# Kernel optimization log

Hardware: AMD Instinct MI355X
Metric: run time of the kernel (lower is better)

## Reference

```python
import jax, jax.numpy as jnp
import numpy as np

N, D = 256, 512
DIST_W, ANGLE_W = 1.0, 2.0
EPS_PD = 1e-6    # F.pairwise_distance eps (added to the difference)
EPS_COS = 1e-8   # F.cosine_similarity eps (denominator floor)
CLAMP = 1e-7     # acos clamp margin


def _smooth_l1(x):
    # F.smooth_l1_loss with beta=1.0, elementwise (reduction handled by caller)
    ax = jnp.abs(x)
    return jnp.where(ax < 1.0, 0.5 * ax * ax, ax - 0.5)


def _pairwise_dist(E):
    # Faithful to the looped version: dist[i,j] = ||e_i - e_j + eps|| for i<j,
    # mirrored to the lower triangle, zero diagonal.
    diff = E[:, None, :] - E[None, :, :] + EPS_PD          # [n, n, d]
    d = jnp.sqrt(jnp.sum(diff * diff, axis=-1))            # [n, n]
    upper = jnp.triu(d, k=1)
    return upper + upper.T


def _angles(E):
    # ang[j, i, k] = angle at vertex j between (e_i - e_j) and (e_k - e_j)
    Dv = E[None, :, :] - E[:, None, :]                     # Dv[j, a] = e_a - e_j
    norms = jnp.sqrt(jnp.sum(Dv * Dv, axis=-1))            # [n, n]
    dots = jnp.einsum('jad,jbd->jab', Dv, Dv)              # [n, n, n]
    denom = jnp.maximum(norms[:, :, None] * norms[:, None, :], EPS_COS)
    cos = jnp.clip(dots / denom, -1.0 + CLAMP, 1.0 - CLAMP)
    return jnp.arccos(cos)


def setup_inputs() -> dict:
    key = jax.random.key(0)
    k1, k2 = jax.random.split(key)
    return {
        'student_embeddings': jax.random.normal(k1, (N, D), dtype=jnp.float32),
        'teacher_embeddings': jax.random.normal(k2, (N, D), dtype=jnp.float32),
    }


def reference(student_embeddings, teacher_embeddings):
    # distance-wise loss: smooth_l1 mean over the full n x n matrix
    ds = _pairwise_dist(student_embeddings)
    dt = _pairwise_dist(teacher_embeddings)
    distance_loss = jnp.mean(_smooth_l1(ds - dt))

    # angle-wise loss: mean over triplets i<j<k (vertex at j)
    n = student_embeddings.shape[0]
    ang_s = _angles(student_embeddings)
    ang_t = _angles(teacher_embeddings)
    idx = jnp.arange(n)
    # mask[j, i, k] = (i < j) & (j < k)
    mask = (idx[None, :, None] < idx[:, None, None]) & (idx[:, None, None] < idx[None, None, :])
    count = n * (n - 1) * (n - 2) // 6
    angle_loss = jnp.sum(_smooth_l1(ang_s - ang_t) * mask) / count

    total_loss = DIST_W * distance_loss + ANGLE_W * angle_loss
    return (total_loss, distance_loss, angle_loss)
```

## Files before the change

kernel.cpp:

```cpp
#include <hip/hip_runtime.h>
#include <math.h>

#define N 256
#define D 512


__global__ void gram_kernel(const float* __restrict__ Es,
                            const float* __restrict__ Et,
                            float* __restrict__ Gs,
                            float* __restrict__ Gt) {
    const float* E = blockIdx.z ? Et : Es;
    float* G = blockIdx.z ? Gt : Gs;
    __shared__ float As[16][17];
    __shared__ float Bs[16][17];
    const int tx = threadIdx.x, ty = threadIdx.y;
    const int row = blockIdx.y * 16 + ty;
    const int colr = blockIdx.x * 16 + ty;
    float acc = 0.f;
    for (int k0 = 0; k0 < D; k0 += 16) {
        As[ty][tx] = E[row * D + k0 + tx];
        Bs[ty][tx] = E[colr * D + k0 + tx];
        __syncthreads();
#pragma unroll
        for (int kk = 0; kk < 16; ++kk)
            acc += As[ty][kk] * Bs[tx][kk];
        __syncthreads();
    }
    G[row * N + blockIdx.x * 16 + tx] = acc;
}

__global__ void rowsum_kernel(const float* __restrict__ Es,
                              const float* __restrict__ Et,
                              float* __restrict__ Ss,
                              float* __restrict__ St) {
    const float* E = blockIdx.y ? Et : Es;
    float* S = blockIdx.y ? St : Ss;
    const int row = blockIdx.x;
    const int t = threadIdx.x;
    float s = 0.f;
    for (int d = t; d < D; d += 64) s += E[row * D + d];
#pragma unroll
    for (int off = 32; off > 0; off >>= 1) s += __shfl_down(s, off);
    if (t == 0) S[row] = s;
}

__device__ __forceinline__ float smooth_l1(float x) {
    float ax = fabsf(x);
    return ax < 1.f ? 0.5f * ax * ax : ax - 0.5f;
}

__global__ void dist_kernel(const float* __restrict__ Gs,
                            const float* __restrict__ Gt,
                            const float* __restrict__ Ss,
                            const float* __restrict__ St,
                            float* __restrict__ acc) {
    const int i = blockIdx.x;
    const int j = threadIdx.x;
    float v = 0.f;
    if (i < j) {
        const float epsc = (float)((double)D * 1e-12);
        float ds2 = Gs[i * N + i] - 2.f * Gs[i * N + j] + Gs[j * N + j]
                    + 2e-6f * (Ss[i] - Ss[j]) + epsc;
        float dt2 = Gt[i * N + i] - 2.f * Gt[i * N + j] + Gt[j * N + j]
                    + 2e-6f * (St[i] - St[j]) + epsc;
        v = smooth_l1(sqrtf(ds2) - sqrtf(dt2));
    }
    __shared__ float red[256];
    red[j] = v;
    __syncthreads();
    for (int s = 128; s > 0; s >>= 1) {
        if (j < s) red[j] += red[j + s];
        __syncthreads();
    }
    if (j == 0) atomicAdd(&acc[0], red[0]);
}

__global__ void angle_kernel(const float* __restrict__ Gs,
                             const float* __restrict__ Gt,
                             float* __restrict__ acc) {
    const int j = blockIdx.x + 1;
    const int tid = threadIdx.x;
    __shared__ float cs[N], ct[N], rns[N], rnt[N];
    const float Gsjj = Gs[j * N + j];
    const float Gtjj = Gt[j * N + j];

    {
        float cja = Gs[tid * N + j];
        float cjb = Gt[tid * N + j];
        cs[tid] = cja;
        ct[tid] = cjb;
        float n2s = Gs[tid * N + tid] - 2.f * cja + Gsjj;
        float n2t = Gt[tid * N + tid] - 2.f * cjb + Gtjj;
        rns[tid] = (tid == j) ? 0.f : 1.f / sqrtf(n2s);
        rnt[tid] = (tid == j) ? 0.f : 1.f / sqrtf(n2t);
    }
    __syncthreads();

    const int nk = 255 - j;
    const int npairs = j * nk;
    const float lo = (float)(-1.0 + 1e-7);
    const float hi = (float)(1.0 - 1e-7);

    float partial = 0.f;
    for (int p = tid; p < npairs; p += 256) {
        int i = p / nk;
        int k = j + 1 + (p - i * nk);
        float dots = Gs[i * N + k] - cs[i] - cs[k] + Gsjj;
        float dott = Gt[i * N + k] - ct[i] - ct[k] + Gtjj;
        float coss = dots * rns[i] * rns[k];
        float cost = dott * rnt[i] * rnt[k];
        coss = fminf(fmaxf(coss, lo), hi);
        cost = fminf(fmaxf(cost, lo), hi);
        partial += smooth_l1(acosf(coss) - acosf(cost));
    }

    __shared__ float red[256];
    red[tid] = partial;
    __syncthreads();
    for (int s = 128; s > 0; s >>= 1) {
        if (tid < s) red[tid] += red[tid + s];
        __syncthreads();
    }
    if (tid == 0) atomicAdd(&acc[1], red[0]);
}

__global__ void finalize_kernel(const float* __restrict__ acc,
                                float* __restrict__ out) {
    float dl = 2.f * acc[0] / (float)(N * N);
    float al = acc[1] / (float)(N * (N - 1) * (N - 2) / 6);
    out[0] = 1.0f * dl + 2.0f * al;
    out[1] = dl;
    out[2] = al;
}

extern "C" void kernel_launch(void* const* d_in, const int* in_sizes, int n_in,
                              void* d_out, int out_size, void* d_ws, size_t ws_size,
                              hipStream_t stream) {
    const float* Es = (const float*)d_in[0];
    const float* Et = (const float*)d_in[1];
    float* out = (float*)d_out;
    float* ws = (float*)d_ws;

    float* acc = ws;
    float* Gs  = ws + 64;
    float* Gt  = Gs + N * N;
    float* Ss  = Gt + N * N;
    float* St  = Ss + N;

    hipMemsetAsync(acc, 0, 2 * sizeof(float), stream);
    gram_kernel<<<dim3(16, 16, 2), dim3(16, 16), 0, stream>>>(Es, Et, Gs, Gt);
    rowsum_kernel<<<dim3(N, 2), 64, 0, stream>>>(Es, Et, Ss, St);
    dist_kernel<<<N, N, 0, stream>>>(Gs, Gt, Ss, St, acc);
    angle_kernel<<<N - 2, N, 0, stream>>>(Gs, Gt, acc);
    finalize_kernel<<<1, 1, 0, stream>>>(acc, out);
}
```

Measured before the change: 102.9 us.

## Fuse distance loss into angle kernel, split angle work, vectorize gram loads

Computes the distance loss inside the angle kernel from the squared norms it already builds, which removes the rowsum and dist kernels and the memset (the accumulator is now zeroed inside the gram kernel). The angle work for each vertex j is split across 4 blocks to raise parallelism. The integer division is replaced by a float reciprocal with a correction step, and rsqrtf is used. The gram kernel now uses float4 loads and 64-wide K tiles. The tradeoffs are that the 2e-6 eps terms in the pairwise distance are dropped, and zeroing acc inside the gram kernel relies on stream ordering.

After: 87.51 us. 1.18x faster.

```diff
diff --git a/kernel.cpp b/kernel.cpp
--- a/kernel.cpp
+++ b/kernel.cpp
@@ -3,125 +3,117 @@
 
 #define N 256
 #define D 512
-
-
-__global__ void gram_kernel(const float* __restrict__ Es,
-                            const float* __restrict__ Et,
-                            float* __restrict__ Gs,
-                            float* __restrict__ Gt) {
-    const float* E = blockIdx.z ? Et : Es;
-    float* G = blockIdx.z ? Gt : Gs;
-    __shared__ float As[16][17];
-    __shared__ float Bs[16][17];
-    const int tx = threadIdx.x, ty = threadIdx.y;
-    const int row = blockIdx.y * 16 + ty;
-    const int colr = blockIdx.x * 16 + ty;
-    float acc = 0.f;
-    for (int k0 = 0; k0 < D; k0 += 16) {
-        As[ty][tx] = E[row * D + k0 + tx];
-        Bs[ty][tx] = E[colr * D + k0 + tx];
-        __syncthreads();
-#pragma unroll
-        for (int kk = 0; kk < 16; ++kk)
-            acc += As[ty][kk] * Bs[tx][kk];
-        __syncthreads();
-    }
-    G[row * N + blockIdx.x * 16 + tx] = acc;
-}
-
-__global__ void rowsum_kernel(const float* __restrict__ Es,
-                              const float* __restrict__ Et,
-                              float* __restrict__ Ss,
-                              float* __restrict__ St) {
-    const float* E = blockIdx.y ? Et : Es;
-    float* S = blockIdx.y ? St : Ss;
-    const int row = blockIdx.x;
-    const int t = threadIdx.x;
-    float s = 0.f;
-    for (int d = t; d < D; d += 64) s += E[row * D + d];
-#pragma unroll
-    for (int off = 32; off > 0; off >>= 1) s += __shfl_down(s, off);
-    if (t == 0) S[row] = s;
-}
+#define KT 64
+#define LDSPAD 68
+#define SPLIT 4
 
 __device__ __forceinline__ float smooth_l1(float x) {
     float ax = fabsf(x);
     return ax < 1.f ? 0.5f * ax * ax : ax - 0.5f;
 }
 
-__global__ void dist_kernel(const float* __restrict__ Gs,
-                            const float* __restrict__ Gt,
-                            const float* __restrict__ Ss,
-                            const float* __restrict__ St,
-                            float* __restrict__ acc) {
-    const int i = blockIdx.x;
-    const int j = threadIdx.x;
-    float v = 0.f;
-    if (i < j) {
-        const float epsc = (float)((double)D * 1e-12);
-        float ds2 = Gs[i * N + i] - 2.f * Gs[i * N + j] + Gs[j * N + j]
-                    + 2e-6f * (Ss[i] - Ss[j]) + epsc;
-        float dt2 = Gt[i * N + i] - 2.f * Gt[i * N + j] + Gt[j * N + j]
-                    + 2e-6f * (St[i] - St[j]) + epsc;
-        v = smooth_l1(sqrtf(ds2) - sqrtf(dt2));
+__global__ __launch_bounds__(256) void gram_kernel(const float* __restrict__ Es,
+                                                   const float* __restrict__ Et,
+                                                   float* __restrict__ Gs,
+                                                   float* __restrict__ Gt,
+                                                   float* __restrict__ acc) {
+    const float* E = blockIdx.z ? Et : Es;
+    float* G = blockIdx.z ? Gt : Gs;
+    __shared__ __align__(16) float As[16 * LDSPAD];
+    __shared__ __align__(16) float Bs[16 * LDSPAD];
+    const int tx = threadIdx.x, ty = threadIdx.y;
+    const int t = ty * 16 + tx;
+    if (blockIdx.x == 0 && blockIdx.y == 0 && blockIdx.z == 0 && t == 0) {
+        acc[0] = 0.f;
+        acc[1] = 0.f;
     }
-    __shared__ float red[256];
-    red[j] = v;
-    __syncthreads();
-    for (int s = 128; s > 0; s >>= 1) {
-        if (j < s) red[j] += red[j + s];
+    const int lr = t >> 4;
+    const int lc = (t & 15) * 4;
+    const int rowA = blockIdx.y * 16 + lr;
+    const int rowB = blockIdx.x * 16 + lr;
+    float sum = 0.f;
+    for (int k0 = 0; k0 < D; k0 += KT) {
+        float4 a4 = *(const float4*)&E[rowA * D + k0 + lc];
+        float4 b4 = *(const float4*)&E[rowB * D + k0 + lc];
+        *(float4*)&As[lr * LDSPAD + lc] = a4;
+        *(float4*)&Bs[lr * LDSPAD + lc] = b4;
+        __syncthreads();
+        const float4* Ar = (const float4*)&As[ty * LDSPAD];
+        const float4* Br = (const float4*)&Bs[tx * LDSPAD];
+#pragma unroll
+        for (int kk = 0; kk < KT / 4; ++kk) {
+            float4 a = Ar[kk], b = Br[kk];
+            sum += a.x * b.x + a.y * b.y + a.z * b.z + a.w * b.w;
+        }
         __syncthreads();
     }
-    if (j == 0) atomicAdd(&acc[0], red[0]);
+    G[(blockIdx.y * 16 + ty) * N + blockIdx.x * 16 + tx] = sum;
 }
 
-__global__ void angle_kernel(const float* __restrict__ Gs,
-                             const float* __restrict__ Gt,
-                             float* __restrict__ acc) {
+__global__ __launch_bounds__(256) void angle_dist_kernel(const float* __restrict__ Gs,
+                                                         const float* __restrict__ Gt,
+                                                         float* __restrict__ acc) {
     const int j = blockIdx.x + 1;
     const int tid = threadIdx.x;
     __shared__ float cs[N], ct[N], rns[N], rnt[N];
+    __shared__ float2 red[256];
     const float Gsjj = Gs[j * N + j];
     const float Gtjj = Gt[j * N + j];
 
+    float distp = 0.f;
     {
-        float cja = Gs[tid * N + j];
-        float cjb = Gt[tid * N + j];
-        cs[tid] = cja;
-        ct[tid] = cjb;
-        float n2s = Gs[tid * N + tid] - 2.f * cja + Gsjj;
-        float n2t = Gt[tid * N + tid] - 2.f * cjb + Gtjj;
-        rns[tid] = (tid == j) ? 0.f : 1.f / sqrtf(n2s);
-        rnt[tid] = (tid == j) ? 0.f : 1.f / sqrtf(n2t);
+        const int a = tid;
+        float cja = Gs[a * N + j];
+        float cjb = Gt[a * N + j];
+        cs[a] = cja;
+        ct[a] = cjb;
+        float n2s = Gs[a * N + a] - 2.f * cja + Gsjj;
+        float n2t = Gt[a * N + a] - 2.f * cjb + Gtjj;
+        float rs = (a == j) ? 0.f : rsqrtf(n2s);
+        float rt = (a == j) ? 0.f : rsqrtf(n2t);
+        rns[a] = rs;
+        rnt[a] = rt;
+        if (blockIdx.y == 0 && a < j) {
+            distp = smooth_l1(n2s * rs - n2t * rt);
+        }
     }
     __syncthreads();
 
     const int nk = 255 - j;
     const int npairs = j * nk;
-    const float lo = (float)(-1.0 + 1e-7);
-    const float hi = (float)(1.0 - 1e-7);
+    const float inv_nk = 1.0f / (float)nk;
+    const float lo = -0.99999994f;
+    const float hi = 0.99999994f;
 
-    float partial = 0.f;
-    for (int p = tid; p < npairs; p += 256) {
-        int i = p / nk;
-        int k = j + 1 + (p - i * nk);
+    float anglep = 0.f;
+    for (int p = blockIdx.y * 256 + tid; p < npairs; p += 256 * SPLIT) {
+        int i = (int)((float)p * inv_nk);
+        int rem = p - i * nk;
+        if (rem < 0) { --i; rem += nk; }
+        else if (rem >= nk) { ++i; rem -= nk; }
+        const int k = j + 1 + rem;
         float dots = Gs[i * N + k] - cs[i] - cs[k] + Gsjj;
         float dott = Gt[i * N + k] - ct[i] - ct[k] + Gtjj;
-        float coss = dots * rns[i] * rns[k];
-        float cost = dott * rnt[i] * rnt[k];
+        float coss = dots * (rns[i] * rns[k]);
+        float cost = dott * (rnt[i] * rnt[k]);
         coss = fminf(fmaxf(coss, lo), hi);
         cost = fminf(fmaxf(cost, lo), hi);
-        partial += smooth_l1(acosf(coss) - acosf(cost));
+        anglep += smooth_l1(acosf(coss) - acosf(cost));
     }
 
-    __shared__ float red[256];
-    red[tid] = partial;
+    red[tid] = make_float2(distp, anglep);
     __syncthreads();
     for (int s = 128; s > 0; s >>= 1) {
-        if (tid < s) red[tid] += red[tid + s];
+        if (tid < s) {
+            red[tid].x += red[tid + s].x;
+            red[tid].y += red[tid + s].y;
+        }
         __syncthreads();
     }
-    if (tid == 0) atomicAdd(&acc[1], red[0]);
+    if (tid == 0) {
+        atomicAdd(&acc[1], red[0].y);
+        if (blockIdx.y == 0) atomicAdd(&acc[0], red[0].x);
+    }
 }
 
 __global__ void finalize_kernel(const float* __restrict__ acc,
@@ -144,13 +136,8 @@
     float* acc = ws;
     float* Gs  = ws + 64;
     float* Gt  = Gs + N * N;
-    float* Ss  = Gt + N * N;
-    float* St  = Ss + N;
 
-    hipMemsetAsync(acc, 0, 2 * sizeof(float), stream);
-    gram_kernel<<<dim3(16, 16, 2), dim3(16, 16), 0, stream>>>(Es, Et, Gs, Gt);
-    rowsum_kernel<<<dim3(N, 2), 64, 0, stream>>>(Es, Et, Ss, St);
-    dist_kernel<<<N, N, 0, stream>>>(Gs, Gt, Ss, St, acc);
-    angle_kernel<<<N - 2, N, 0, stream>>>(Gs, Gt, acc);
+    gram_kernel<<<dim3(16, 16, 2), dim3(16, 16), 0, stream>>>(Es, Et, Gs, Gt, acc);
+    angle_dist_kernel<<<dim3(N - 1, SPLIT), 256, 0, stream>>>(Gs, Gt, acc);
     finalize_kernel<<<1, 1, 0, stream>>>(acc, out);
 }
```
